# Performance work log

Measured on AMD Instinct MI355X. Metric: run time of the kernel, lower is better.

## Reference

```python
import jax, jax.numpy as jnp
import numpy as np

B, L, H = 32, 4096, 1024

def setup_inputs() -> dict:
    key = jax.random.key(0)
    k1, k2, k3, k4 = jax.random.split(key, 4)
    hidden = jax.random.normal(k1, (1, B, H), dtype=jnp.float32)
    targets = jax.random.normal(k2, (B, L, H), dtype=jnp.float32)
    # nn.Linear(H, H): weight [H, H], bias [H]
    W = jax.random.normal(k3, (H, H), dtype=jnp.float32) * (1.0 / np.sqrt(H))
    b = jax.random.normal(k4, (H,), dtype=jnp.float32) * 0.01
    return {"hidden": hidden, "targets": targets, "W": W, "b": b}

def reference(hidden, targets, W, b):
    # hidden: [1, B, H] -> h: [B, H]
    h = hidden[0]
    # 'general' score: energy = Linear(target) = target @ W.T + b; score = dot(h_b, energy)
    energy = jnp.einsum('blh,gh->blg', targets, W) + b          # [B, L, H]
    attn_energies = jnp.einsum('blh,bh->bl', energy, h)          # [B, L]
    return jax.nn.softmax(attn_energies, axis=1)[:, None, :]     # [B, 1, L]
```

## Files before the change

### kernel.cpp

```cpp
#include <hip/hip_runtime.h>
#include <math.h>

constexpr int B_ = 32;
constexpr int L_ = 4096;
constexpr int H_ = 1024;

constexpr int GSPLIT = 8;
constexpr int GCHUNK = H_ / GSPLIT;

__global__ __launch_bounds__(256) void vW_kernel(const float* __restrict__ hidden,
                                                 const float* __restrict__ W,
                                                 float* __restrict__ v) {
    const int b  = blockIdx.x;
    const int hc = blockIdx.y;
    const int gs = blockIdx.z;
    const int t  = threadIdx.x;
    const int h  = hc * 256 + t;

    __shared__ float hlds[GCHUNK];
    if (t < GCHUNK) hlds[t] = hidden[b * H_ + gs * GCHUNK + t];
    __syncthreads();

    const float* Wp = W + (size_t)(gs * GCHUNK) * H_ + h;
    float acc = 0.f;
#pragma unroll 16
    for (int g = 0; g < GCHUNK; ++g) {
        acc = fmaf(hlds[g], Wp[(size_t)g * H_], acc);
    }
    atomicAdd(&v[b * H_ + h], acc);
}

__global__ __launch_bounds__(256) void energy_kernel(const float* __restrict__ targets,
                                                     const float* __restrict__ v,
                                                     float* __restrict__ e) {
    const int blocksPerB = L_ / 4;
    const int b  = blockIdx.x / blocksPerB;
    const int lc = blockIdx.x % blocksPerB;
    const int t  = threadIdx.x;

    __shared__ float4 vlds[H_ / 4];
    vlds[t] = reinterpret_cast<const float4*>(v + (size_t)b * H_)[t];
    __syncthreads();

    const int wave = t >> 6;
    const int lane = t & 63;
    const int l = lc * 4 + wave;

    const float4* row =
        reinterpret_cast<const float4*>(targets + ((size_t)b * L_ + l) * H_);

    float acc = 0.f;
#pragma unroll
    for (int k = 0; k < 4; ++k) {
        const float4 tv = row[lane + 64 * k];
        const float4 vv = vlds[lane + 64 * k];
        acc = fmaf(tv.x, vv.x, acc);
        acc = fmaf(tv.y, vv.y, acc);
        acc = fmaf(tv.z, vv.z, acc);
        acc = fmaf(tv.w, vv.w, acc);
    }
#pragma unroll
    for (int m = 32; m >= 1; m >>= 1) acc += __shfl_xor(acc, m, 64);
    if (lane == 0) e[(size_t)b * L_ + l] = acc;
}

__global__ __launch_bounds__(256) void softmax_kernel(const float* __restrict__ e,
                                                      float* __restrict__ out) {
    const int b = blockIdx.x;
    const int t = threadIdx.x;
    const int wave = t >> 6;
    const int lane = t & 63;

    const float4* ep = reinterpret_cast<const float4*>(e + (size_t)b * L_);
    float4 x[4];
    float mx = -INFINITY;
#pragma unroll
    for (int k = 0; k < 4; ++k) {
        x[k] = ep[t + 256 * k];
        mx = fmaxf(mx, fmaxf(fmaxf(x[k].x, x[k].y), fmaxf(x[k].z, x[k].w)));
    }

    __shared__ float redmax[4];
    __shared__ float redsum[4];

#pragma unroll
    for (int m = 32; m >= 1; m >>= 1) mx = fmaxf(mx, __shfl_xor(mx, m, 64));
    if (lane == 0) redmax[wave] = mx;
    __syncthreads();
    mx = fmaxf(fmaxf(redmax[0], redmax[1]), fmaxf(redmax[2], redmax[3]));

    float s = 0.f;
#pragma unroll
    for (int k = 0; k < 4; ++k) {
        x[k].x = expf(x[k].x - mx);
        x[k].y = expf(x[k].y - mx);
        x[k].z = expf(x[k].z - mx);
        x[k].w = expf(x[k].w - mx);
        s += x[k].x + x[k].y + x[k].z + x[k].w;
    }
#pragma unroll
    for (int m = 32; m >= 1; m >>= 1) s += __shfl_xor(s, m, 64);
    if (lane == 0) redsum[wave] = s;
    __syncthreads();
    s = redsum[0] + redsum[1] + redsum[2] + redsum[3];

    const float inv = 1.f / s;
    float4* op = reinterpret_cast<float4*>(out + (size_t)b * L_);
#pragma unroll
    for (int k = 0; k < 4; ++k) {
        float4 y = x[k];
        y.x *= inv; y.y *= inv; y.z *= inv; y.w *= inv;
        op[t + 256 * k] = y;
    }
}

extern "C" void kernel_launch(void* const* d_in, const int* in_sizes, int n_in,
                              void* d_out, int out_size, void* d_ws, size_t ws_size,
                              hipStream_t stream) {
    const float* hidden  = (const float*)d_in[0];
    const float* targets = (const float*)d_in[1];
    const float* W       = (const float*)d_in[2];
    float* out = (float*)d_out;

    float* v = (float*)d_ws;
    float* e = v + (size_t)B_ * H_;

    hipMemsetAsync(v, 0, (size_t)B_ * H_ * sizeof(float), stream);
    vW_kernel<<<dim3(B_, H_ / 256, GSPLIT), 256, 0, stream>>>(hidden, W, v);
    energy_kernel<<<dim3(B_ * L_ / 4), 256, 0, stream>>>(targets, v, e);
    softmax_kernel<<<dim3(B_), 256, 0, stream>>>(e, out);
}
```

Before: 687.3 us.

## Drop split-K atomics in vW and process four rows per wave in energy

The vW kernel now reduces over the full hidden dimension per thread and writes the result directly, which removes the memset and the atomic adds. The energy kernel now has each wave handle four target rows, with the v vector held in registers, so more loads are in flight and there are fewer blocks. The trade-off is a vW grid of only 128 blocks with long serial dependent loops, which may leave the GPU underused.

```diff
diff --git a/kernel.cpp b/kernel.cpp
--- a/kernel.cpp
+++ b/kernel.cpp
@@ -5,35 +5,35 @@
 constexpr int L_ = 4096;
 constexpr int H_ = 1024;
 
-constexpr int GSPLIT = 8;
-constexpr int GCHUNK = H_ / GSPLIT;
 
 __global__ __launch_bounds__(256) void vW_kernel(const float* __restrict__ hidden,
                                                  const float* __restrict__ W,
                                                  float* __restrict__ v) {
     const int b  = blockIdx.x;
     const int hc = blockIdx.y;
-    const int gs = blockIdx.z;
     const int t  = threadIdx.x;
     const int h  = hc * 256 + t;
 
-    __shared__ float hlds[GCHUNK];
-    if (t < GCHUNK) hlds[t] = hidden[b * H_ + gs * GCHUNK + t];
+    __shared__ float hlds[H_];
+    reinterpret_cast<float4*>(hlds)[t] =
+        reinterpret_cast<const float4*>(hidden + (size_t)b * H_)[t];
     __syncthreads();
 
-    const float* Wp = W + (size_t)(gs * GCHUNK) * H_ + h;
+    const float* Wp = W + h;
     float acc = 0.f;
 #pragma unroll 16
-    for (int g = 0; g < GCHUNK; ++g) {
+    for (int g = 0; g < H_; ++g) {
         acc = fmaf(hlds[g], Wp[(size_t)g * H_], acc);
     }
-    atomicAdd(&v[b * H_ + h], acc);
+    v[b * H_ + h] = acc;
 }
+
+constexpr int ROWS_PER_BLOCK = 16;
 
 __global__ __launch_bounds__(256) void energy_kernel(const float* __restrict__ targets,
                                                      const float* __restrict__ v,
                                                      float* __restrict__ e) {
-    const int blocksPerB = L_ / 4;
+    const int blocksPerB = L_ / ROWS_PER_BLOCK;
     const int b  = blockIdx.x / blocksPerB;
     const int lc = blockIdx.x % blocksPerB;
     const int t  = threadIdx.x;
@@ -44,24 +44,35 @@
 
     const int wave = t >> 6;
     const int lane = t & 63;
-    const int l = lc * 4 + wave;
+    const int l0 = lc * ROWS_PER_BLOCK + wave * 4;
 
-    const float4* row =
-        reinterpret_cast<const float4*>(targets + ((size_t)b * L_ + l) * H_);
+    float4 vv[4];
+#pragma unroll
+    for (int k = 0; k < 4; ++k) vv[k] = vlds[lane + 64 * k];
 
-    float acc = 0.f;
+    const float4* base =
+        reinterpret_cast<const float4*>(targets + ((size_t)b * L_ + l0) * H_);
+
+    float acc[4] = {0.f, 0.f, 0.f, 0.f};
 #pragma unroll
-    for (int k = 0; k < 4; ++k) {
-        const float4 tv = row[lane + 64 * k];
-        const float4 vv = vlds[lane + 64 * k];
-        acc = fmaf(tv.x, vv.x, acc);
-        acc = fmaf(tv.y, vv.y, acc);
-        acc = fmaf(tv.z, vv.z, acc);
-        acc = fmaf(tv.w, vv.w, acc);
+    for (int r = 0; r < 4; ++r) {
+#pragma unroll
+        for (int k = 0; k < 4; ++k) {
+            const float4 tv = base[r * 256 + lane + 64 * k];
+            acc[r] = fmaf(tv.x, vv[k].x, acc[r]);
+            acc[r] = fmaf(tv.y, vv[k].y, acc[r]);
+            acc[r] = fmaf(tv.z, vv[k].z, acc[r]);
+            acc[r] = fmaf(tv.w, vv[k].w, acc[r]);
+        }
     }
+
 #pragma unroll
-    for (int m = 32; m >= 1; m >>= 1) acc += __shfl_xor(acc, m, 64);
-    if (lane == 0) e[(size_t)b * L_ + l] = acc;
+    for (int r = 0; r < 4; ++r) {
+        float a = acc[r];
+#pragma unroll
+        for (int m = 32; m >= 1; m >>= 1) a += __shfl_xor(a, m, 64);
+        if (lane == 0) e[(size_t)b * L_ + l0 + r] = a;
+    }
 }
 
 __global__ __launch_bounds__(256) void softmax_kernel(const float* __restrict__ e,
@@ -125,8 +136,7 @@
     float* v = (float*)d_ws;
     float* e = v + (size_t)B_ * H_;
 
-    hipMemsetAsync(v, 0, (size_t)B_ * H_ * sizeof(float), stream);
-    vW_kernel<<<dim3(B_, H_ / 256, GSPLIT), 256, 0, stream>>>(hidden, W, v);
-    energy_kernel<<<dim3(B_ * L_ / 4), 256, 0, stream>>>(targets, v, e);
+    vW_kernel<<<dim3(B_, H_ / 256), 256, 0, stream>>>(hidden, W, v);
+    energy_kernel<<<dim3(B_ * L_ / ROWS_PER_BLOCK), 256, 0, stream>>>(targets, v, e);
     softmax_kernel<<<dim3(B_), 256, 0, stream>>>(e, out);
 }
```

Result: slower. 716.6 us (+4.3%).
